# Performance work log

Measured on AMD Instinct MI355X. Metric: run time of the kernel, lower is better.

The kernel has to match this reference:

```python
import jax, jax.numpy as jnp
import numpy as np

B, S, D, H, K, L, NS, NT = 32, 512, 1024, 512, 16, 16, 16, 16
SMOOTH = 0.1
EPS = 1e-8


def setup_inputs() -> dict:
    key = jax.random.key(0)
    ks = jax.random.split(key, 16)
    hidden_layers = jax.random.normal(ks[0], (B, S, D), jnp.float32)
    span_start = jax.random.randint(ks[1], (B, K), 0, S - L).astype(jnp.int32)
    span_idx = span_start[..., None] + jnp.arange(L, dtype=jnp.int32)  # [B,K,L] in-range
    span_mask = jnp.ones((B, K, L), jnp.float32)
    span_end = span_start + (L - 1)
    length = jnp.full((B,), S, jnp.int32)
    slot_emb = jax.random.normal(ks[2], (B, K, D), jnp.float32)
    tgt_slot_embs = jax.random.normal(ks[3], (NT, D), jnp.float32)
    src_slot_ids = jax.random.randint(ks[4], (B, K), 0, NS).astype(jnp.int32)
    sc = 0.02
    p = {
        'Wih_f': jax.random.normal(ks[5], (4 * H, D)) * sc,
        'Whh_f': jax.random.normal(ks[6], (4 * H, H)) * sc,
        'bih_f': jnp.zeros((4 * H,)), 'bhh_f': jnp.zeros((4 * H,)),
        'Wih_b': jax.random.normal(ks[7], (4 * H, D)) * sc,
        'Whh_b': jax.random.normal(ks[8], (4 * H, H)) * sc,
        'bih_b': jnp.zeros((4 * H,)), 'bhh_b': jnp.zeros((4 * H,)),
        # slot_name_projection_for_slot / _for_context are eye-initialized with zero bias
        'Wps1': jnp.eye(D), 'bps1': jnp.zeros((D,)),
        'Wps2': jnp.eye(D), 'bps2': jnp.zeros((D,)),
        'Wpc1': jnp.eye(D), 'bpc1': jnp.zeros((D,)),
        'Wpc2': jnp.eye(D), 'bpc2': jnp.zeros((D,)),
    }
    inp = dict(hidden_layers=hidden_layers, span_idx=span_idx, span_mask=span_mask,
               span_start=span_start, span_end=span_end, length=length,
               slot_emb=slot_emb, tgt_slot_embs=tgt_slot_embs, src_slot_ids=src_slot_ids)
    inp.update(p)
    return inp


def _lstm_dir(x, m, Wih, Whh, bih, bhh):
    # x: [N,L,D], m: [N,L]; masked steps carry state through, emit 0
    N = x.shape[0]
    h0 = jnp.zeros((N, H), x.dtype)
    c0 = jnp.zeros((N, H), x.dtype)

    def step(carry, xm):
        h, c = carry
        xt, mt = xm
        g = xt @ Wih.T + h @ Whh.T + (bih + bhh)
        i, f, gg, o = jnp.split(g, 4, axis=-1)  # torch gate order i,f,g,o
        cn = jax.nn.sigmoid(f) * c + jax.nn.sigmoid(i) * jnp.tanh(gg)
        hn = jax.nn.sigmoid(o) * jnp.tanh(cn)
        mt = mt[:, None]
        h = mt * hn + (1.0 - mt) * h
        c = mt * cn + (1.0 - mt) * c
        return (h, c), h * mt

    _, ys = jax.lax.scan(step, (h0, c0), (jnp.swapaxes(x, 0, 1), m.T))
    return jnp.swapaxes(ys, 0, 1)  # [N,L,H]


def _mlp(x, W1, b1, W2, b2):
    # Linear -> Tanh -> (Dropout eval=identity) -> Linear
    return jnp.tanh(x @ W1.T + b1) @ W2.T + b2


def reference(hidden_layers, span_idx, span_mask, span_start, span_end, length,
              slot_emb, tgt_slot_embs, src_slot_ids,
              Wih_f, Whh_f, bih_f, bhh_f, Wih_b, Whh_b, bih_b, bhh_b,
              Wps1, bps1, Wps2, bps2, Wpc1, bpc1, Wpc2, bpc2):
    # gather span tokens: [B,K,L,D]
    spans = hidden_layers[jnp.arange(B)[:, None, None], span_idx]
    x = spans.reshape(B * K, L, D)
    m = span_mask.reshape(B * K, L)
    hf = _lstm_dir(x, m, Wih_f, Whh_f, bih_f, bhh_f)
    hb = _lstm_dir(x[:, ::-1], m[:, ::-1], Wih_b, Whh_b, bih_b, bhh_b)[:, ::-1]
    out = jnp.concatenate([hf, hb], axis=-1)           # [BK,L,2H]
    slot_feats = out.sum(axis=1).reshape(B, K, 2 * H)  # sum-pool over span

    # context attention (faithful to source: returns attn @ hidden, no softmax)
    sf = jax.lax.stop_gradient(slot_feats)
    pos = jnp.arange(S)
    cmask = (pos[None, None, :] < span_start[..., None]) | \
            ((pos[None, None, :] > span_end[..., None]) & (pos[None, None, :] < length[:, None, None]))
    attn = jnp.einsum('bkd,bsd->bks', sf, hidden_layers) * cmask.astype(hidden_layers.dtype)
    context = jnp.einsum('bks,bsd->bkd', attn, hidden_layers)  # [B,K,D]

    # smooth labels via projected slot-name embeddings (all detached in source)
    s_cat = jnp.concatenate([_mlp(slot_emb, Wps1, bps1, Wps2, bps2),
                             _mlp(slot_emb, Wpc1, bpc1, Wpc2, bpc2)], axis=-1)  # [B,K,2D]
    t_cat = jnp.concatenate([_mlp(tgt_slot_embs, Wps1, bps1, Wps2, bps2),
                             _mlp(tgt_slot_embs, Wpc1, bpc1, Wpc2, bpc2)], axis=-1)  # [NT,2D]
    s_cat = jax.lax.stop_gradient(s_cat)
    t_cat = jax.lax.stop_gradient(t_cat)
    sn = jnp.maximum(jnp.linalg.norm(s_cat, axis=-1), EPS)
    tn = jnp.maximum(jnp.linalg.norm(t_cat, axis=-1), EPS)
    sim = jnp.einsum('bkd,td->bkt', s_cat, t_cat) / (sn[..., None] * tn[None, None, :])
    sim = sim / sim.sum(axis=-1, keepdims=True) * (1.0 - SMOOTH)
    one_hot = jax.nn.one_hot(src_slot_ids, NS, dtype=sim.dtype) * SMOOTH
    labels = jnp.concatenate([one_hot, sim], axis=-1)  # [B,K,NS+NT]

    return jnp.concatenate([slot_feats, context, labels], axis=-1)  # [B,K,2H+D+NS+NT]
```

## Files before the change

### kernel.cpp

```cpp
#include <hip/hip_runtime.h>
#include <cstdio>

#define B_ 32
#define S_ 512
#define D_ 1024
#define H_ 512
#define K_ 16
#define L_ 16
#define NT_ 16
#define NSEQ 512
#define XROWS 8192
#define G4H 2048
#define OUTC 2080
#define MROWS 528

typedef unsigned short u16;
typedef __bf16 bf16x8 __attribute__((ext_vector_type(8)));
typedef float f32x4 __attribute__((ext_vector_type(4)));

__device__ inline u16 f2b(float f) {
  union { float f; unsigned u; } x; x.f = f;
  unsigned r = x.u + 0x7FFFu + ((x.u >> 16) & 1u);
  return (u16)(r >> 16);
}
__device__ inline float b2f(u16 h) {
  union { unsigned u; float f; } c; c.u = ((unsigned)h) << 16;
  return c.f;
}
__device__ inline float sigf(float x) { return 1.0f / (1.0f + expf(-x)); }
__device__ inline float wredsum(float v) {
#pragma unroll
  for (int off = 32; off > 0; off >>= 1) v += __shfl_xor(v, off);
  return v;
}
__device__ inline void gl16(const u16* g, u16* l) {
  __builtin_amdgcn_global_load_lds(
      (const __attribute__((address_space(1))) unsigned int*)g,
      (__attribute__((address_space(3))) unsigned int*)l, 16, 0, 0);
}

__device__ inline int swzidx(int R, int c) {
  return (R >> 1) * 64 + (((((R & 1) << 2) | c) ^ ((R >> 1) & 7)) << 3);
}
__device__ inline void stage_map(int wave, int lane, int j, int& lrow, int& cu) {
  int sr = j * 32 + wave * 8 + (lane >> 3);
  int ci = (lane & 7) ^ (sr & 7);
  lrow = sr * 2 + (ci >> 2);
  cu = (ci & 3) * 8;
}

__global__ __launch_bounds__(256) void split_kernel(const float* __restrict__ in,
                                                    u16* __restrict__ hi,
                                                    u16* __restrict__ lo, int n) {
  int i = blockIdx.x * 256 + threadIdx.x;
  if (i >= n) return;
  float x = in[i];
  u16 h = f2b(x);
  hi[i] = h;
  lo[i] = f2b(x - b2f(h));
}

__global__ __launch_bounds__(256) void hsplit_kernel(const float* __restrict__ in,
                                                     u16* __restrict__ hi,
                                                     u16* __restrict__ lo) {
  size_t i = ((size_t)blockIdx.x * 256 + threadIdx.x) * 4;
  float4 v = *reinterpret_cast<const float4*>(in + i);
  float a[4] = {v.x, v.y, v.z, v.w};
#pragma unroll
  for (int j = 0; j < 4; ++j) {
    u16 h = f2b(a[j]);
    hi[i + j] = h;
    lo[i + j] = f2b(a[j] - b2f(h));
  }
}

__global__ __launch_bounds__(256) void icast_kernel(const float* __restrict__ W,
                                                    u16* __restrict__ out, int Kd) {
  int rp = blockIdx.x;
  int j = rp >> 2, g = rp & 3;
  const float* src = W + ((size_t)(g * H_ + j)) * Kd;
  u16* dst = out + (size_t)rp * Kd;
  for (int k = threadIdx.x; k < Kd; k += 256) dst[k] = f2b(src[k]);
}

__global__ __launch_bounds__(256) void bsum_kernel(const float* __restrict__ bih,
                                                   const float* __restrict__ bhh,
                                                   float* __restrict__ bsum) {
  int rp = blockIdx.x * 256 + threadIdx.x;
  if (rp >= G4H) return;
  int j = rp >> 2, g = rp & 3;
  bsum[rp] = bih[g * H_ + j] + bhh[g * H_ + j];
}

__global__ __launch_bounds__(256) void big_gemm_kernel(
    const u16* __restrict__ Hh, const int* __restrict__ span_idx,
    const u16* __restrict__ Wih2, u16* __restrict__ G2) {
  __shared__ u16 As[2][128 * 32];
  __shared__ u16 Bs[2][128 * 32];
  const int tid = threadIdx.x;
  const int bn = blockIdx.x * 128, bm = blockIdx.y * 128;
  const int wave = tid >> 6, lane = tid & 63;
  const int wm = (wave >> 1) * 64, wn = (wave & 1) * 64;
  const int fr = lane & 15;
  const int cc = lane >> 4;

  const u16* asrc[2];
  const u16* bsrc[2];
  int doff[2];
#pragma unroll
  for (int j = 0; j < 2; ++j) {
    int lrow, cu;
    stage_map(wave, lane, j, lrow, cu);
    int gr = bm + lrow;
    int b = gr >> 8;
    int sidx = span_idx[gr];
    asrc[j] = Hh + ((size_t)(b * S_ + sidx)) * D_ + cu;
    bsrc[j] = Wih2 + (size_t)(bn + lrow) * D_ + cu;
    doff[j] = (j * 256 + wave * 64) * 8;
  }
  int aoff[4], boff[4];
#pragma unroll
  for (int m = 0; m < 4; ++m) aoff[m] = swzidx(wm + m * 16 + fr, cc);
#pragma unroll
  for (int n = 0; n < 4; ++n) boff[n] = swzidx(wn + n * 16 + fr, cc);

  f32x4 acc[4][4] = {};
  auto STAGE = [&](int buf, int k0) {
    gl16(asrc[0] + k0, &As[buf][doff[0]]);
    gl16(asrc[1] + k0, &As[buf][doff[1]]);
    gl16(bsrc[0] + k0, &Bs[buf][doff[0]]);
    gl16(bsrc[1] + k0, &Bs[buf][doff[1]]);
  };
  STAGE(0, 0);
  int cur = 0;
  for (int k0 = 0; k0 < D_; k0 += 32) {
    if (k0 + 32 < D_) {
      STAGE(cur ^ 1, k0 + 32);
      asm volatile("s_waitcnt vmcnt(4)" ::: "memory");
    } else {
      asm volatile("s_waitcnt vmcnt(0)" ::: "memory");
    }
    __builtin_amdgcn_s_barrier();
    bf16x8 af[4], bfr[4];
#pragma unroll
    for (int m = 0; m < 4; ++m) af[m] = *reinterpret_cast<const bf16x8*>(&As[cur][aoff[m]]);
#pragma unroll
    for (int n = 0; n < 4; ++n) bfr[n] = *reinterpret_cast<const bf16x8*>(&Bs[cur][boff[n]]);
#pragma unroll
    for (int m = 0; m < 4; ++m)
#pragma unroll
      for (int n = 0; n < 4; ++n)
        acc[m][n] = __builtin_amdgcn_mfma_f32_16x16x32_bf16(af[m], bfr[n], acc[m][n], 0, 0, 0);
    __builtin_amdgcn_s_barrier();
    cur ^= 1;
  }
  const int ci = lane & 15;
  const int r0 = (lane >> 4) * 4;
#pragma unroll
  for (int m = 0; m < 4; ++m)
#pragma unroll
    for (int n = 0; n < 4; ++n) {
      int col = bn + wn + n * 16 + ci;
#pragma unroll
      for (int r = 0; r < 4; ++r) {
        int row = bm + wm + m * 16 + r0 + r;
        size_t g2row = (size_t)(row & 15) * NSEQ + (row >> 4);
        G2[g2row * 4096 + col] = f2b(acc[m][n][r]);
      }
    }
}

__global__ __launch_bounds__(256) void lstm_step_kernel(
    const u16* __restrict__ hbf_in,
    const u16* __restrict__ Whhf, const u16* __restrict__ Whhb,
    const u16* __restrict__ G2,
    const float* __restrict__ bsumf, const float* __restrict__ bsumb,
    const float* __restrict__ mask,
    float* __restrict__ hst, float* __restrict__ cst,
    u16* __restrict__ hbf_out,
    float* __restrict__ sf,
    int t, int first) {
  __shared__ u16 As[2][64 * 32];
  __shared__ u16 Bs[2][64 * 32];
  const int tid = threadIdx.x;
  const int bz = blockIdx.z;
  const int treal = bz ? (L_ - 1 - t) : t;
  const u16* Whh = bz ? Whhb : Whhf;
  const float* bsum = bz ? bsumb : bsumf;
  const size_t sofs = (size_t)bz * NSEQ * H_;
  const int bm = blockIdx.y * 64, bn = blockIdx.x * 64;
  const int wave = tid >> 6, lane = tid & 63;
  const int wm = (wave >> 1) * 32, wn = (wave & 1) * 32;
  f32x4 acc[2][2] = {};
  const int fr = lane & 15;
  const int cc = lane >> 4;

  if (!first) {
    int lrow, cu;
    stage_map(wave, lane, 0, lrow, cu);
    const u16* asrc = hbf_in + sofs + (size_t)(bm + lrow) * H_ + cu;
    const u16* bsrc = Whh + (size_t)(bn + lrow) * H_ + cu;
    const int doff = wave * 64 * 8;
    int aoff[2], boff[2];
#pragma unroll
    for (int m = 0; m < 2; ++m) aoff[m] = swzidx(wm + m * 16 + fr, cc);
#pragma unroll
    for (int n = 0; n < 2; ++n) boff[n] = swzidx(wn + n * 16 + fr, cc);

    auto STAGE = [&](int buf, int k0) {
      gl16(asrc + k0, &As[buf][doff]);
      gl16(bsrc + k0, &Bs[buf][doff]);
    };
    STAGE(0, 0);
    int cur = 0;
    for (int k0 = 0; k0 < H_; k0 += 32) {
      if (k0 + 32 < H_) {
        STAGE(cur ^ 1, k0 + 32);
        asm volatile("s_waitcnt vmcnt(2)" ::: "memory");
      } else {
        asm volatile("s_waitcnt vmcnt(0)" ::: "memory");
      }
      __builtin_amdgcn_s_barrier();
      bf16x8 af[2], bfr[2];
#pragma unroll
      for (int m = 0; m < 2; ++m) af[m] = *reinterpret_cast<const bf16x8*>(&As[cur][aoff[m]]);
#pragma unroll
      for (int n = 0; n < 2; ++n) bfr[n] = *reinterpret_cast<const bf16x8*>(&Bs[cur][boff[n]]);
#pragma unroll
      for (int m = 0; m < 2; ++m)
#pragma unroll
        for (int n = 0; n < 2; ++n)
          acc[m][n] = __builtin_amdgcn_mfma_f32_16x16x32_bf16(af[m], bfr[n], acc[m][n], 0, 0, 0);
      __builtin_amdgcn_s_barrier();
      cur ^= 1;
    }
  }

  const int ci = lane & 15;
  const int r0 = (lane >> 4) * 4;
  const int q = lane & 3;
#pragma unroll
  for (int m = 0; m < 2; ++m)
#pragma unroll
    for (int n = 0; n < 2; ++n) {
      int c = bn + wn + n * 16 + ci;
      int rowbase = bm + wm + m * 16 + r0;
      float val[4];
#pragma unroll
      for (int r = 0; r < 4; ++r) {
        int nrow = rowbase + r;
        float g2 = b2f(G2[((size_t)treal * NSEQ + nrow) * 4096 + (size_t)bz * 2048 + c]);
        val[r] = acc[m][n][r] + g2 + bsum[c];
      }
      float x1[4], x2[4], x3[4];
#pragma unroll
      for (int r = 0; r < 4; ++r) {
        x1[r] = __shfl_xor(val[r], 1);
        x2[r] = __shfl_xor(val[r], 2);
        x3[r] = __shfl_xor(x1[r], 2);
      }
      if (q == 0) {
        int j = c >> 2;
#pragma unroll
        for (int r = 0; r < 4; ++r) {
          int nrow = rowbase + r;
          float gi = val[r], gf = x1[r], gg = x2[r], go = x3[r];
          float mv = mask[nrow * L_ + treal];
          size_t sidx = sofs + (size_t)nrow * H_ + j;
          float co = first ? 0.f : cst[sidx];
          float ho = first ? 0.f : hst[sidx];
          float cn = sigf(gf) * co + sigf(gi) * tanhf(gg);
          float hn = sigf(go) * tanhf(cn);
          float hnew = mv * hn + (1.f - mv) * ho;
          float cnew = mv * cn + (1.f - mv) * co;
          hst[sidx] = hnew;
          cst[sidx] = cnew;
          hbf_out[sidx] = f2b(hnew);
          size_t fidx = (size_t)nrow * 1024 + bz * 512 + j;
          float contrib = hnew * mv;
          if (first) sf[fidx] = contrib;
          else sf[fidx] += contrib;
        }
      }
    }
}

__global__ __launch_bounds__(256) void copy_sf_split_kernel(const float* __restrict__ sf,
                                                            float* __restrict__ out,
                                                            u16* __restrict__ sfh,
                                                            u16* __restrict__ sfl) {
  int bk = blockIdx.x;
  for (int d = threadIdx.x; d < 1024; d += 256) {
    size_t i = (size_t)bk * 1024 + d;
    float v = sf[i];
    out[(size_t)bk * OUTC + d] = v;
    u16 h = f2b(v);
    sfh[i] = h;
    sfl[i] = f2b(v - b2f(h));
  }
}

__global__ __launch_bounds__(256) void attn_mfma_kernel(
    const u16* __restrict__ sfh, const u16* __restrict__ sfl,
    const u16* __restrict__ Hh, const u16* __restrict__ Hl,
    const int* __restrict__ sstart, const int* __restrict__ send,
    const int* __restrict__ len,
    float* __restrict__ attn_f) {
  __shared__ u16 Bh[128 * 32];
  __shared__ u16 Bl[128 * 32];
  const int b = blockIdx.x;
  const int s0 = blockIdx.y * 128;
  const int tid = threadIdx.x;
  const int wave = tid >> 6, lane = tid & 63;
  const int fr = lane & 15;
  const int cc = lane >> 4;
  const int kg = cc * 8;
  f32x4 acc[2] = {};

  const u16* hsrc[2];
  const u16* lsrc[2];
  int doff[2];
#pragma unroll
  for (int j = 0; j < 2; ++j) {
    int lrow, cu;
    stage_map(wave, lane, j, lrow, cu);
    size_t goff = ((size_t)b * S_ + s0 + lrow) * D_ + cu;
    hsrc[j] = Hh + goff;
    lsrc[j] = Hl + goff;
    doff[j] = (j * 256 + wave * 64) * 8;
  }
  int boff[2];
#pragma unroll
  for (int nt = 0; nt < 2; ++nt) boff[nt] = swzidx(wave * 32 + nt * 16 + fr, cc);

  for (int k0 = 0; k0 < D_; k0 += 32) {
    gl16(hsrc[0] + k0, &Bh[doff[0]]);
    gl16(hsrc[1] + k0, &Bh[doff[1]]);
    gl16(lsrc[0] + k0, &Bl[doff[0]]);
    gl16(lsrc[1] + k0, &Bl[doff[1]]);
    __syncthreads();
    size_t aoff = ((size_t)b * 16 + fr) * D_ + k0 + kg;
    bf16x8 ah = *reinterpret_cast<const bf16x8*>(sfh + aoff);
    bf16x8 al = *reinterpret_cast<const bf16x8*>(sfl + aoff);
#pragma unroll
    for (int nt = 0; nt < 2; ++nt) {
      bf16x8 bh = *reinterpret_cast<const bf16x8*>(&Bh[boff[nt]]);
      bf16x8 bl = *reinterpret_cast<const bf16x8*>(&Bl[boff[nt]]);
      acc[nt] = __builtin_amdgcn_mfma_f32_16x16x32_bf16(ah, bh, acc[nt], 0, 0, 0);
      acc[nt] = __builtin_amdgcn_mfma_f32_16x16x32_bf16(ah, bl, acc[nt], 0, 0, 0);
      acc[nt] = __builtin_amdgcn_mfma_f32_16x16x32_bf16(al, bh, acc[nt], 0, 0, 0);
    }
    __syncthreads();
  }
  const int ln = len[b];
#pragma unroll
  for (int nt = 0; nt < 2; ++nt) {
    int s = s0 + wave * 32 + nt * 16 + (lane & 15);
#pragma unroll
    for (int r = 0; r < 4; ++r) {
      int krow = (lane >> 4) * 4 + r;
      int bk = b * 16 + krow;
      int st = sstart[bk], en = send[bk];
      bool cm = (s < st) || ((s > en) && (s < ln));
      attn_f[(size_t)bk * S_ + s] = cm ? acc[nt][r] : 0.f;
    }
  }
}

__global__ __launch_bounds__(256) void ctx_f32_kernel(
    const float* __restrict__ attn_f, const float* __restrict__ hidden,
    float* __restrict__ out) {
  __shared__ float att[16 * 512];
  const int b = blockIdx.x;
  const int d0 = blockIdx.y * 128;
  const int tid = threadIdx.x;
  for (int i = tid; i < 16 * 512; i += 256)
    att[i] = attn_f[((size_t)b * 16 + (i >> 9)) * S_ + (i & 511)];
  __syncthreads();
  const int d = d0 + (tid & 127);
  const int sh = tid >> 7;
  float acc[16] = {};
  const float* hp = hidden + ((size_t)b * S_ + sh * 256) * D_ + d;
  for (int s = 0; s < 256; ++s) {
    float hv = hp[(size_t)s * D_];
    int si = sh * 256 + s;
#pragma unroll
    for (int kr = 0; kr < 16; ++kr) acc[kr] += att[kr * 512 + si] * hv;
  }
  __syncthreads();
  float* red = att;
#pragma unroll
  for (int kr = 0; kr < 16; ++kr) red[(sh * 16 + kr) * 128 + (tid & 127)] = acc[kr];
  __syncthreads();
  if (sh == 0) {
#pragma unroll
    for (int kr = 0; kr < 16; ++kr)
      out[((size_t)b * 16 + kr) * OUTC + 1024 + d] =
          red[kr * 128 + (tid & 127)] + red[(16 + kr) * 128 + (tid & 127)];
  }
}

__global__ __launch_bounds__(256) void mlp_gemm_kernel(
    const u16* __restrict__ Ah, const u16* __restrict__ Al, int a_br_stride,
    const u16* __restrict__ B0h, const u16* __restrict__ B0l,
    const u16* __restrict__ B1h, const u16* __restrict__ B1l,
    float* __restrict__ P, int M) {
  __shared__ u16 Ash[2][64 * 32];
  __shared__ u16 Asl[2][64 * 32];
  __shared__ u16 Bsh[2][64 * 32];
  __shared__ u16 Bsl[2][64 * 32];
  const int tid = threadIdx.x;
  const int zz = blockIdx.z;
  const int br = zz >> 2, ks = zz & 3;
  const u16* Ah_ = Ah + (size_t)br * a_br_stride;
  const u16* Al_ = Al + (size_t)br * a_br_stride;
  const u16* Bh = br ? B1h : B0h;
  const u16* Bl = br ? B1l : B0l;
  const int bm = blockIdx.y * 64, bn = blockIdx.x * 64;
  const int wave = tid >> 6, lane = tid & 63;
  const int wm = (wave >> 1) * 32, wn = (wave & 1) * 32;
  f32x4 acc[2][2] = {};
  const int fr = lane & 15;
  const int cc = lane >> 4;

  int lrow, cu;
  stage_map(wave, lane, 0, lrow, cu);
  int ga = bm + lrow;
  if (ga >= M) ga = M - 1;
  const u16* ahsrc = Ah_ + (size_t)ga * D_ + cu;
  const u16* alsrc = Al_ + (size_t)ga * D_ + cu;
  const u16* bhsrc = Bh + (size_t)(bn + lrow) * D_ + cu;
  const u16* blsrc = Bl + (size_t)(bn + lrow) * D_ + cu;
  const int doff = wave * 64 * 8;
  int aoff[2], boff[2];
#pragma unroll
  for (int m = 0; m < 2; ++m) aoff[m] = swzidx(wm + m * 16 + fr, cc);
#pragma unroll
  for (int n = 0; n < 2; ++n) boff[n] = swzidx(wn + n * 16 + fr, cc);

  auto STAGE = [&](int buf, int k0) {
    gl16(ahsrc + k0, &Ash[buf][doff]);
    gl16(alsrc + k0, &Asl[buf][doff]);
    gl16(bhsrc + k0, &Bsh[buf][doff]);
    gl16(blsrc + k0, &Bsl[buf][doff]);
  };
  const int kbeg = ks * 256;
  STAGE(0, kbeg);
  int cur = 0;
  for (int k0 = kbeg; k0 < kbeg + 256; k0 += 32) {
    if (k0 + 32 < kbeg + 256) {
      STAGE(cur ^ 1, k0 + 32);
      asm volatile("s_waitcnt vmcnt(4)" ::: "memory");
    } else {
      asm volatile("s_waitcnt vmcnt(0)" ::: "memory");
    }
    __builtin_amdgcn_s_barrier();
    bf16x8 afh[2], afl[2], bfh[2], bfl[2];
#pragma unroll
    for (int m = 0; m < 2; ++m) {
      afh[m] = *reinterpret_cast<const bf16x8*>(&Ash[cur][aoff[m]]);
      afl[m] = *reinterpret_cast<const bf16x8*>(&Asl[cur][aoff[m]]);
    }
#pragma unroll
    for (int n = 0; n < 2; ++n) {
      bfh[n] = *reinterpret_cast<const bf16x8*>(&Bsh[cur][boff[n]]);
      bfl[n] = *reinterpret_cast<const bf16x8*>(&Bsl[cur][boff[n]]);
    }
#pragma unroll
    for (int m = 0; m < 2; ++m)
#pragma unroll
      for (int n = 0; n < 2; ++n) {
        acc[m][n] = __builtin_amdgcn_mfma_f32_16x16x32_bf16(afh[m], bfh[n], acc[m][n], 0, 0, 0);
        acc[m][n] = __builtin_amdgcn_mfma_f32_16x16x32_bf16(afh[m], bfl[n], acc[m][n], 0, 0, 0);
        acc[m][n] = __builtin_amdgcn_mfma_f32_16x16x32_bf16(afl[m], bfh[n], acc[m][n], 0, 0, 0);
      }
    __builtin_amdgcn_s_barrier();
    cur ^= 1;
  }
  const int ci = lane & 15;
  const int r0 = (lane >> 4) * 4;
#pragma unroll
  for (int m = 0; m < 2; ++m)
#pragma unroll
    for (int n = 0; n < 2; ++n) {
      int col = bn + wn + n * 16 + ci;
#pragma unroll
      for (int r = 0; r < 4; ++r) {
        int row = bm + wm + m * 16 + r0 + r;
        if (row < M)
          P[((size_t)zz * MROWS + row) * D_ + col] = acc[m][n][r];
      }
    }
}

__global__ __launch_bounds__(256) void mlp_reduce_kernel(
    const float* __restrict__ P,
    const float* __restrict__ bias0, const float* __restrict__ bias1,
    u16* __restrict__ Oh, u16* __restrict__ Ol,
    float* __restrict__ Cf,
    int mode) {
  int i = blockIdx.x * 256 + threadIdx.x;
  int e = i * 4;
  const int per_br = MROWS * D_;
  int br = e / per_br;
  int rem = e - br * per_br;
  int row = rem >> 10;
  int col = rem & 1023;
  float4 s = {0.f, 0.f, 0.f, 0.f};
#pragma unroll
  for (int ks = 0; ks < 4; ++ks) {
    float4 v = *reinterpret_cast<const float4*>(
        P + ((size_t)(br * 4 + ks) * MROWS + row) * D_ + col);
    s.x += v.x; s.y += v.y; s.z += v.z; s.w += v.w;
  }
  const float* bias = br ? bias1 : bias0;
  s.x += bias[col]; s.y += bias[col + 1]; s.z += bias[col + 2]; s.w += bias[col + 3];
  if (mode == 0) {
    float a[4] = {tanhf(s.x), tanhf(s.y), tanhf(s.z), tanhf(s.w)};
    size_t o = (size_t)br * per_br + (size_t)row * D_ + col;
#pragma unroll
    for (int j = 0; j < 4; ++j) {
      u16 h = f2b(a[j]);
      Oh[o + j] = h;
      Ol[o + j] = f2b(a[j] - b2f(h));
    }
  } else {
    *reinterpret_cast<float4*>(Cf + (size_t)row * 2048 + br * 1024 + col) = s;
  }
}

__global__ __launch_bounds__(64) void labels_kernel(
    const float* __restrict__ s_cat, const float* __restrict__ t_cat,
    const int* __restrict__ src_ids, float* __restrict__ out) {
  int bk = blockIdx.x, lane = threadIdx.x;
  const float* srow = s_cat + (size_t)bk * 2048;
  float np = 0.f;
  float dots[16], tsq[16];
#pragma unroll
  for (int t = 0; t < 16; ++t) { dots[t] = 0.f; tsq[t] = 0.f; }
  for (int j = lane; j < 2048; j += 64) {
    float sv = srow[j];
    np += sv * sv;
#pragma unroll
    for (int t = 0; t < 16; ++t) {
      float tv = t_cat[t * 2048 + j];
      dots[t] += sv * tv;
      tsq[t] += tv * tv;
    }
  }
  np = wredsum(np);
#pragma unroll
  for (int t = 0; t < 16; ++t) { dots[t] = wredsum(dots[t]); tsq[t] = wredsum(tsq[t]); }
  float sn = fmaxf(sqrtf(np), 1e-8f);
  float ssum = 0.f;
  float sims[16];
#pragma unroll
  for (int t = 0; t < 16; ++t) {
    float tn = fmaxf(sqrtf(tsq[t]), 1e-8f);
    sims[t] = dots[t] / (sn * tn);
    ssum += sims[t];
  }
  float scale = 0.9f / ssum;
  if (lane < 16) {
    out[(size_t)bk * OUTC + 2064 + lane] = sims[lane] * scale;
  } else if (lane < 32) {
    int t2 = lane - 16;
    out[(size_t)bk * OUTC + 2048 + t2] = (src_ids[bk] == t2) ? 0.1f : 0.f;
  }
}

extern "C" void kernel_launch(void* const* d_in, const int* in_sizes, int n_in,
                              void* d_out, int out_size, void* d_ws, size_t ws_size,
                              hipStream_t stream) {
  const float* hidden    = (const float*)d_in[0];
  const int*   span_idx  = (const int*)d_in[1];
  const float* span_mask = (const float*)d_in[2];
  const int*   span_start= (const int*)d_in[3];
  const int*   span_end  = (const int*)d_in[4];
  const int*   length    = (const int*)d_in[5];
  const float* slot_emb  = (const float*)d_in[6];
  const float* tgt       = (const float*)d_in[7];
  const int*   src_ids   = (const int*)d_in[8];
  const float* Wih_f = (const float*)d_in[9];
  const float* Whh_f = (const float*)d_in[10];
  const float* bih_f = (const float*)d_in[11];
  const float* bhh_f = (const float*)d_in[12];
  const float* Wih_b = (const float*)d_in[13];
  const float* Whh_b = (const float*)d_in[14];
  const float* bih_b = (const float*)d_in[15];
  const float* bhh_b = (const float*)d_in[16];
  const float* Wps1 = (const float*)d_in[17];
  const float* bps1 = (const float*)d_in[18];
  const float* Wps2 = (const float*)d_in[19];
  const float* bps2 = (const float*)d_in[20];
  const float* Wpc1 = (const float*)d_in[21];
  const float* bpc1 = (const float*)d_in[22];
  const float* Wpc2 = (const float*)d_in[23];
  const float* bpc2 = (const float*)d_in[24];
  float* out = (float*)d_out;

  char* p = (char*)d_ws;
  auto alloc = [&](size_t bytes) -> void* {
    void* r = (void*)p;
    p += (bytes + 255) & ~(size_t)255;
    return r;
  };
  char*  BIG1  = (char*)alloc((size_t)XROWS * 4096 * 2);
  char*  BIG2  = (char*)alloc((size_t)2 * B_ * S_ * D_ * 2);
  float* hst   = (float*)alloc((size_t)2 * NSEQ * H_ * 4);
  float* cst   = (float*)alloc((size_t)2 * NSEQ * H_ * 4);
  u16*   hbfA  = (u16*)alloc((size_t)2 * NSEQ * H_ * 2);
  u16*   hbfB  = (u16*)alloc((size_t)2 * NSEQ * H_ * 2);
  float* sf    = (float*)alloc((size_t)NSEQ * 1024 * 4);
  u16*   sfh   = (u16*)alloc((size_t)NSEQ * 1024 * 2);
  u16*   sfl   = (u16*)alloc((size_t)NSEQ * 1024 * 2);
  float* attn_f= (float*)alloc((size_t)NSEQ * S_ * 4);
  float* CAT   = (float*)alloc((size_t)MROWS * 2048 * 4);
  u16* Wih2_i = (u16*)alloc((size_t)2 * G4H * D_ * 2);
  u16* Whhf_i = (u16*)alloc((size_t)G4H * H_ * 2);
  u16* Whhb_i = (u16*)alloc((size_t)G4H * H_ * 2);
  float* bsumf = (float*)alloc(G4H * 4);
  float* bsumb = (float*)alloc(G4H * 4);
  u16* W1sh = (u16*)alloc((size_t)D_ * D_ * 2); u16* W1sl = (u16*)alloc((size_t)D_ * D_ * 2);
  u16* W2sh = (u16*)alloc((size_t)D_ * D_ * 2); u16* W2sl = (u16*)alloc((size_t)D_ * D_ * 2);
  u16* W1ch = (u16*)alloc((size_t)D_ * D_ * 2); u16* W1cl = (u16*)alloc((size_t)D_ * D_ * 2);
  u16* W2ch = (u16*)alloc((size_t)D_ * D_ * 2); u16* W2cl = (u16*)alloc((size_t)D_ * D_ * 2);
  u16* SEh = (u16*)alloc((size_t)MROWS * D_ * 2); u16* SEl = (u16*)alloc((size_t)MROWS * D_ * 2);
  u16* T1h = (u16*)alloc((size_t)2 * MROWS * D_ * 2);
  u16* T1l = (u16*)alloc((size_t)2 * MROWS * D_ * 2);

  u16*   G2 = (u16*)BIG1;
  float* P  = (float*)BIG1;
  u16*   Hh = (u16*)BIG2;
  u16*   Hl = Hh + (size_t)B_ * S_ * D_;

  size_t need = (size_t)(p - (char*)d_ws);
  if (need > ws_size) {
    fprintf(stderr, "kernel_launch: ws too small, need %zu have %zu\n", need, ws_size);
    return;
  }

  auto split = [&](const float* src, u16* hi, u16* lo, int n) {
    split_kernel<<<(n + 255) / 256, 256, 0, stream>>>(src, hi, lo, n);
  };

  icast_kernel<<<G4H, 256, 0, stream>>>(Wih_f, Wih2_i, D_);
  icast_kernel<<<G4H, 256, 0, stream>>>(Wih_b, Wih2_i + (size_t)G4H * D_, D_);
  icast_kernel<<<G4H, 256, 0, stream>>>(Whh_f, Whhf_i, H_);
  icast_kernel<<<G4H, 256, 0, stream>>>(Whh_b, Whhb_i, H_);
  bsum_kernel<<<8, 256, 0, stream>>>(bih_f, bhh_f, bsumf);
  bsum_kernel<<<8, 256, 0, stream>>>(bih_b, bhh_b, bsumb);
  split(Wps1, W1sh, W1sl, D_ * D_);
  split(Wps2, W2sh, W2sl, D_ * D_);
  split(Wpc1, W1ch, W1cl, D_ * D_);
  split(Wpc2, W2ch, W2cl, D_ * D_);
  split(slot_emb, SEh, SEl, NSEQ * D_);
  split(tgt, SEh + (size_t)NSEQ * D_, SEl + (size_t)NSEQ * D_, NT_ * D_);

  hsplit_kernel<<<(B_ * S_ * D_) / (4 * 256), 256, 0, stream>>>(hidden, Hh, Hl);

  {
    dim3 g(4096 / 128, XROWS / 128);
    big_gemm_kernel<<<g, 256, 0, stream>>>(Hh, span_idx, Wih2_i, G2);
  }

  for (int t = 0; t < L_; ++t) {
    const u16* hin = (t & 1) ? hbfA : hbfB;
    u16* hout = (t & 1) ? hbfB : hbfA;
    dim3 g(G4H / 64, NSEQ / 64, 2);
    lstm_step_kernel<<<g, 256, 0, stream>>>(hin, Whhf_i, Whhb_i, G2, bsumf, bsumb,
                                            span_mask, hst, cst, hout, sf,
                                            t, t == 0 ? 1 : 0);
  }

  copy_sf_split_kernel<<<NSEQ, 256, 0, stream>>>(sf, out, sfh, sfl);

  {
    dim3 g(B_, S_ / 128);
    attn_mfma_kernel<<<g, 256, 0, stream>>>(sfh, sfl, Hh, Hl,
                                            span_start, span_end, length, attn_f);
  }
  {
    dim3 g(B_, D_ / 128);
    ctx_f32_kernel<<<g, 256, 0, stream>>>(attn_f, hidden, out);
  }

  {
    dim3 g(D_ / 64, (MROWS + 63) / 64, 8);
    dim3 rg((2 * MROWS * D_) / (4 * 256));
    mlp_gemm_kernel<<<g, 256, 0, stream>>>(SEh, SEl, 0, W1sh, W1sl, W1ch, W1cl, P, MROWS);
    mlp_reduce_kernel<<<rg, 256, 0, stream>>>(P, bps1, bpc1, T1h, T1l, nullptr, 0);
    mlp_gemm_kernel<<<g, 256, 0, stream>>>(T1h, T1l, MROWS * D_, W2sh, W2sl, W2ch, W2cl, P, MROWS);
    mlp_reduce_kernel<<<rg, 256, 0, stream>>>(P, bps2, bpc2, nullptr, nullptr, CAT, 1);
  }

  const float* t_cat = CAT + (size_t)NSEQ * 2048;
  labels_kernel<<<NSEQ, 64, 0, stream>>>(CAT, t_cat, src_ids, out);
}
```

Before: 644.3 us.

## Triple-buffer GEMM LDS stages, reorder big GEMM rows, merge weight splits

The big GEMM, the LSTM step GEMM and the MLP GEMM move from double to triple-buffered LDS staging. This removes one barrier per k-iteration and keeps two loads in flight. The big GEMM now orders its rows time-major, so each output row is written contiguously instead of through a scattered G2 row index. The four projection-weight split launches are merged into a single launch. The cost is extra shared memory per block, which may reduce occupancy.

```diff
diff --git a/kernel.cpp b/kernel.cpp
--- a/kernel.cpp
+++ b/kernel.cpp
@@ -60,6 +60,23 @@
   lo[i] = f2b(x - b2f(h));
 }
 
+__global__ __launch_bounds__(256) void split4_kernel(
+    const float* __restrict__ s0, const float* __restrict__ s1,
+    const float* __restrict__ s2, const float* __restrict__ s3,
+    u16* __restrict__ h0, u16* __restrict__ l0,
+    u16* __restrict__ h1, u16* __restrict__ l1,
+    u16* __restrict__ h2, u16* __restrict__ l2,
+    u16* __restrict__ h3, u16* __restrict__ l3) {
+  const float* src = blockIdx.y == 0 ? s0 : blockIdx.y == 1 ? s1 : blockIdx.y == 2 ? s2 : s3;
+  u16* hi = blockIdx.y == 0 ? h0 : blockIdx.y == 1 ? h1 : blockIdx.y == 2 ? h2 : h3;
+  u16* lo = blockIdx.y == 0 ? l0 : blockIdx.y == 1 ? l1 : blockIdx.y == 2 ? l2 : l3;
+  int i = blockIdx.x * 256 + threadIdx.x;
+  float x = src[i];
+  u16 h = f2b(x);
+  hi[i] = h;
+  lo[i] = f2b(x - b2f(h));
+}
+
 __global__ __launch_bounds__(256) void hsplit_kernel(const float* __restrict__ in,
                                                      u16* __restrict__ hi,
                                                      u16* __restrict__ lo) {
@@ -95,8 +112,8 @@
 __global__ __launch_bounds__(256) void big_gemm_kernel(
     const u16* __restrict__ Hh, const int* __restrict__ span_idx,
     const u16* __restrict__ Wih2, u16* __restrict__ G2) {
-  __shared__ u16 As[2][128 * 32];
-  __shared__ u16 Bs[2][128 * 32];
+  __shared__ u16 As[3][128 * 32];
+  __shared__ u16 Bs[3][128 * 32];
   const int tid = threadIdx.x;
   const int bn = blockIdx.x * 128, bm = blockIdx.y * 128;
   const int wave = tid >> 6, lane = tid & 63;
@@ -112,8 +129,10 @@
     int lrow, cu;
     stage_map(wave, lane, j, lrow, cu);
     int gr = bm + lrow;
-    int b = gr >> 8;
-    int sidx = span_idx[gr];
+    int t = gr >> 9;
+    int seq = gr & 511;
+    int b = seq >> 4;
+    int sidx = span_idx[seq * L_ + t];
     asrc[j] = Hh + ((size_t)(b * S_ + sidx)) * D_ + cu;
     bsrc[j] = Wih2 + (size_t)(bn + lrow) * D_ + cu;
     doff[j] = (j * 256 + wave * 64) * 8;
@@ -131,16 +150,15 @@
     gl16(bsrc[0] + k0, &Bs[buf][doff[0]]);
     gl16(bsrc[1] + k0, &Bs[buf][doff[1]]);
   };
+  const int NK = D_ / 32;
   STAGE(0, 0);
-  int cur = 0;
-  for (int k0 = 0; k0 < D_; k0 += 32) {
-    if (k0 + 32 < D_) {
-      STAGE(cur ^ 1, k0 + 32);
-      asm volatile("s_waitcnt vmcnt(4)" ::: "memory");
-    } else {
-      asm volatile("s_waitcnt vmcnt(0)" ::: "memory");
-    }
+  STAGE(1, 32);
+  for (int j = 0; j < NK; ++j) {
+    if (j + 1 < NK) asm volatile("s_waitcnt vmcnt(4)" ::: "memory");
+    else            asm volatile("s_waitcnt vmcnt(0)" ::: "memory");
     __builtin_amdgcn_s_barrier();
+    if (j + 2 < NK) STAGE((j + 2) % 3, (j + 2) * 32);
+    const int cur = j % 3;
     bf16x8 af[4], bfr[4];
 #pragma unroll
     for (int m = 0; m < 4; ++m) af[m] = *reinterpret_cast<const bf16x8*>(&As[cur][aoff[m]]);
@@ -151,8 +169,6 @@
 #pragma unroll
       for (int n = 0; n < 4; ++n)
         acc[m][n] = __builtin_amdgcn_mfma_f32_16x16x32_bf16(af[m], bfr[n], acc[m][n], 0, 0, 0);
-    __builtin_amdgcn_s_barrier();
-    cur ^= 1;
   }
   const int ci = lane & 15;
   const int r0 = (lane >> 4) * 4;
@@ -164,8 +180,7 @@
 #pragma unroll
       for (int r = 0; r < 4; ++r) {
         int row = bm + wm + m * 16 + r0 + r;
-        size_t g2row = (size_t)(row & 15) * NSEQ + (row >> 4);
-        G2[g2row * 4096 + col] = f2b(acc[m][n][r]);
+        G2[(size_t)row * 4096 + col] = f2b(acc[m][n][r]);
       }
     }
 }
@@ -180,8 +195,8 @@
     u16* __restrict__ hbf_out,
     float* __restrict__ sf,
     int t, int first) {
-  __shared__ u16 As[2][64 * 32];
-  __shared__ u16 Bs[2][64 * 32];
+  __shared__ u16 As[3][64 * 32];
+  __shared__ u16 Bs[3][64 * 32];
   const int tid = threadIdx.x;
   const int bz = blockIdx.z;
   const int treal = bz ? (L_ - 1 - t) : t;
@@ -211,16 +226,15 @@
       gl16(asrc + k0, &As[buf][doff]);
       gl16(bsrc + k0, &Bs[buf][doff]);
     };
+    const int NK = H_ / 32;
     STAGE(0, 0);
-    int cur = 0;
-    for (int k0 = 0; k0 < H_; k0 += 32) {
-      if (k0 + 32 < H_) {
-        STAGE(cur ^ 1, k0 + 32);
-        asm volatile("s_waitcnt vmcnt(2)" ::: "memory");
-      } else {
-        asm volatile("s_waitcnt vmcnt(0)" ::: "memory");
-      }
+    STAGE(1, 32);
+    for (int j = 0; j < NK; ++j) {
+      if (j + 1 < NK) asm volatile("s_waitcnt vmcnt(2)" ::: "memory");
+      else            asm volatile("s_waitcnt vmcnt(0)" ::: "memory");
       __builtin_amdgcn_s_barrier();
+      if (j + 2 < NK) STAGE((j + 2) % 3, (j + 2) * 32);
+      const int cur = j % 3;
       bf16x8 af[2], bfr[2];
 #pragma unroll
       for (int m = 0; m < 2; ++m) af[m] = *reinterpret_cast<const bf16x8*>(&As[cur][aoff[m]]);
@@ -231,8 +245,6 @@
 #pragma unroll
         for (int n = 0; n < 2; ++n)
           acc[m][n] = __builtin_amdgcn_mfma_f32_16x16x32_bf16(af[m], bfr[n], acc[m][n], 0, 0, 0);
-      __builtin_amdgcn_s_barrier();
-      cur ^= 1;
     }
   }
 
@@ -405,10 +417,10 @@
     const u16* __restrict__ B0h, const u16* __restrict__ B0l,
     const u16* __restrict__ B1h, const u16* __restrict__ B1l,
     float* __restrict__ P, int M) {
-  __shared__ u16 Ash[2][64 * 32];
-  __shared__ u16 Asl[2][64 * 32];
-  __shared__ u16 Bsh[2][64 * 32];
-  __shared__ u16 Bsl[2][64 * 32];
+  __shared__ u16 Ash[3][64 * 32];
+  __shared__ u16 Asl[3][64 * 32];
+  __shared__ u16 Bsh[3][64 * 32];
+  __shared__ u16 Bsl[3][64 * 32];
   const int tid = threadIdx.x;
   const int zz = blockIdx.z;
   const int br = zz >> 2, ks = zz & 3;
@@ -445,16 +457,15 @@
     gl16(blsrc + k0, &Bsl[buf][doff]);
   };
   const int kbeg = ks * 256;
+  const int NK = 8;
   STAGE(0, kbeg);
-  int cur = 0;
-  for (int k0 = kbeg; k0 < kbeg + 256; k0 += 32) {
-    if (k0 + 32 < kbeg + 256) {
-      STAGE(cur ^ 1, k0 + 32);
-      asm volatile("s_waitcnt vmcnt(4)" ::: "memory");
-    } else {
-      asm volatile("s_waitcnt vmcnt(0)" ::: "memory");
-    }
+  STAGE(1, kbeg + 32);
+  for (int j = 0; j < NK; ++j) {
+    if (j + 1 < NK) asm volatile("s_waitcnt vmcnt(4)" ::: "memory");
+    else            asm volatile("s_waitcnt vmcnt(0)" ::: "memory");
     __builtin_amdgcn_s_barrier();
+    if (j + 2 < NK) STAGE((j + 2) % 3, kbeg + (j + 2) * 32);
+    const int cur = j % 3;
     bf16x8 afh[2], afl[2], bfh[2], bfl[2];
 #pragma unroll
     for (int m = 0; m < 2; ++m) {
@@ -474,8 +485,6 @@
         acc[m][n] = __builtin_amdgcn_mfma_f32_16x16x32_bf16(afh[m], bfl[n], acc[m][n], 0, 0, 0);
         acc[m][n] = __builtin_amdgcn_mfma_f32_16x16x32_bf16(afl[m], bfh[n], acc[m][n], 0, 0, 0);
       }
-    __builtin_amdgcn_s_barrier();
-    cur ^= 1;
   }
   const int ci = lane & 15;
   const int r0 = (lane >> 4) * 4;
@@ -650,10 +659,12 @@
   icast_kernel<<<G4H, 256, 0, stream>>>(Whh_b, Whhb_i, H_);
   bsum_kernel<<<8, 256, 0, stream>>>(bih_f, bhh_f, bsumf);
   bsum_kernel<<<8, 256, 0, stream>>>(bih_b, bhh_b, bsumb);
-  split(Wps1, W1sh, W1sl, D_ * D_);
-  split(Wps2, W2sh, W2sl, D_ * D_);
-  split(Wpc1, W1ch, W1cl, D_ * D_);
-  split(Wpc2, W2ch, W2cl, D_ * D_);
+  {
+    dim3 g((D_ * D_) / 256, 4);
+    split4_kernel<<<g, 256, 0, stream>>>(Wps1, Wps2, Wpc1, Wpc2,
+                                         W1sh, W1sl, W2sh, W2sl,
+                                         W1ch, W1cl, W2ch, W2cl);
+  }
   split(slot_emb, SEh, SEl, NSEQ * D_);
   split(tgt, SEh + (size_t)NSEQ * D_, SEl + (size_t)NSEQ * D_, NT_ * D_);
 
```

New measurement: 662.7 us. 1.03x slower.
